# Performance work log

Hardware: AMD Instinct MI355X
Metric: run time of the kernel (lower is better)

The kernel has to match this reference:

```python
import jax, jax.numpy as jnp
import numpy as np

B, S, D, H, E = 2, 2048, 1024, 2048, 8
TOP_K = 2
AUX_COEF = 0.01


def setup_inputs() -> dict:
    key = jax.random.key(0)
    ks = jax.random.split(key, 5)
    x = jax.random.normal(ks[0], (B, S, D), jnp.float32)
    Wr = jax.random.normal(ks[1], (E, D), jnp.float32) * 0.02   # router: Linear(D, E) weight [E, D]
    W1 = jax.random.normal(ks[2], (E, H, D), jnp.float32) * 0.02  # per-expert Linear(D, H)
    W2 = jax.random.normal(ks[3], (E, D, H), jnp.float32) * 0.02  # per-expert Linear(H, D)
    W3 = jax.random.normal(ks[4], (E, H, D), jnp.float32) * 0.02  # per-expert Linear(D, H)
    return {"x": x, "Wr": Wr, "W1": W1, "W2": W2, "W3": W3}


def reference(x, Wr, W1, W2, W3):
    b, s, d = x.shape
    e = Wr.shape[0]
    xf = x.reshape(-1, d)                               # [N, D]
    logits = xf @ Wr.T                                  # [N, E]
    probs = jax.nn.softmax(logits, axis=-1)
    _, topk_idx = jax.lax.top_k(logits, TOP_K)          # indices from logits (as in torch code)
    topk_probs, _ = jax.lax.top_k(probs, TOP_K)         # values from probs (same order; softmax monotone)
    # aux loss: density of top-1 expert * mean router prob
    density = jnp.mean(jax.nn.one_hot(topk_idx[:, 0], e, dtype=xf.dtype), axis=0)
    aux_loss = AUX_COEF * jnp.sum(density * probs.mean(axis=0)) * e
    # combine gates: gate[n, j] = sum_i topk_probs[n,i] * 1[topk_idx[n,i]==j]
    gates = jnp.sum(jax.nn.one_hot(topk_idx, e, dtype=xf.dtype) * topk_probs[..., None], axis=1)  # [N, E]
    # dense per-expert SwiGLU; masked combine gives identical math to gather/scatter loop
    h = jax.nn.silu(jnp.einsum('nd,ehd->enh', xf, W1)) * jnp.einsum('nd,ehd->enh', xf, W3)  # [E, N, H]
    y = jnp.einsum('enh,edh->end', h, W2)               # [E, N, D]
    out = jnp.einsum('ne,end->nd', gates, y)            # [N, D]
    return out.reshape(b, s, d), aux_loss
```

## Files before the change

kernel.cpp:

```cpp
#include <hip/hip_runtime.h>
#include <stdint.h>

#define NTOK 4096
#define DD 1024
#define HH 2048
#define NE 8
#define CAP 4096

typedef short bf16x8 __attribute__((ext_vector_type(8)));
typedef float f32x4 __attribute__((ext_vector_type(4)));
typedef unsigned short u16;
typedef unsigned int u32;

__device__ __forceinline__ u16 f2b(float f){
    union { float f; u32 u; } v; v.f = f;
    return (u16)((v.u + 0x7fffu + ((v.u >> 16) & 1u)) >> 16);
}
__device__ __forceinline__ float b2f(u16 h){
    union { u32 u; float f; } v; v.u = ((u32)h) << 16;
    return v.f;
}
__device__ __forceinline__ u32 pk2(float a, float b){
    return (u32)f2b(a) | ((u32)f2b(b) << 16);
}
__device__ __forceinline__ void gload16(const u16* g, u16* l){
    __builtin_amdgcn_global_load_lds((const __attribute__((address_space(1))) u32*)g,
                                     (__attribute__((address_space(3))) u32*)l, 16, 0, 0);
}
__device__ __forceinline__ int prefix_off(const int* __restrict__ cnt, int e){
    int o = 0;
    #pragma unroll
    for (int i = 0; i < NE; ++i) if (i < e) o += cnt[i];
    return o;
}

__global__ __launch_bounds__(256) void prep_kernel(const float* __restrict__ x,
        const float* __restrict__ Wr,
        const float* __restrict__ W1, const float* __restrict__ W3,
        u16* __restrict__ xb, u16* __restrict__ w1b, u16* __restrict__ w3b,
        int* __restrict__ cnt, int* __restrict__ list,
        float* __restrict__ glist, float* __restrict__ psum,
        int* __restrict__ cnt1, int* __restrict__ islot){
    __shared__ float wS[NE * DD];
    __shared__ float psumS[NE];
    __shared__ int cnt1S[NE], cntS[NE], baseS[NE];
    __shared__ int tE[32], tL[32];
    __shared__ float tP[32];
    int tid = threadIdx.x;
    int bid = blockIdx.x;

    if (bid >= 256){
        int cb = bid - 256;
        int m = cb >> 10, blk = cb & 1023;
        const float* s = (m == 0) ? W1 : W3;
        u16* d = (m == 0) ? w1b : w3b;
        int base = blk * 4096 + tid;
        #pragma unroll 4
        for (int j = 0; j < 16; ++j){
            int i = base + j * 256;
            float4 v = reinterpret_cast<const float4*>(s)[i];
            ushort4 o; o.x = f2b(v.x); o.y = f2b(v.y); o.z = f2b(v.z); o.w = f2b(v.w);
            reinterpret_cast<ushort4*>(d)[i] = o;
        }
        return;
    }

    for (int i = tid; i < NE * DD / 4; i += 256)
        reinterpret_cast<float4*>(wS)[i] = reinterpret_cast<const float4*>(Wr)[i];
    if (tid < NE){ psumS[tid] = 0.f; cnt1S[tid] = 0; cntS[tid] = 0; }
    __syncthreads();
    int lane = tid & 63, w = tid >> 6;
    for (int t = 0; t < 4; ++t){
        int li = w * 4 + t;
        int n = bid * 16 + li;
        const float4* xr = reinterpret_cast<const float4*>(x + (size_t)n * DD);
        ushort4* xbr = reinterpret_cast<ushort4*>(xb + (size_t)n * DD);
        float acc[NE];
        #pragma unroll
        for (int e = 0; e < NE; ++e) acc[e] = 0.f;
        #pragma unroll
        for (int j = 0; j < 4; ++j){
            float4 xv = xr[lane + 64 * j];
            ushort4 xo; xo.x = f2b(xv.x); xo.y = f2b(xv.y); xo.z = f2b(xv.z); xo.w = f2b(xv.w);
            xbr[lane + 64 * j] = xo;
            #pragma unroll
            for (int e = 0; e < NE; ++e){
                float4 wv = reinterpret_cast<const float4*>(wS + e * DD)[lane + 64 * j];
                acc[e] += xv.x * wv.x + xv.y * wv.y + xv.z * wv.z + xv.w * wv.w;
            }
        }
        #pragma unroll
        for (int e = 0; e < NE; ++e){
            float v = acc[e];
            #pragma unroll
            for (int s = 32; s > 0; s >>= 1) v += __shfl_xor(v, s);
            acc[e] = v;
        }
        if (lane == 0){
            float mx = acc[0];
            #pragma unroll
            for (int e = 1; e < NE; ++e) mx = fmaxf(mx, acc[e]);
            float p[NE], sm = 0.f;
            #pragma unroll
            for (int e = 0; e < NE; ++e){ p[e] = expf(acc[e] - mx); sm += p[e]; }
            float inv = 1.f / sm;
            #pragma unroll
            for (int e = 0; e < NE; ++e){ p[e] *= inv; atomicAdd(&psumS[e], p[e]); }
            int i0 = 0;
            #pragma unroll
            for (int e = 1; e < NE; ++e) if (acc[e] > acc[i0]) i0 = e;
            int i1 = -1;
            #pragma unroll
            for (int e = 0; e < NE; ++e) if (e != i0 && (i1 < 0 || acc[e] > acc[i1])) i1 = e;
            atomicAdd(&cnt1S[i0], 1);
            int l0 = atomicAdd(&cntS[i0], 1);
            int l1 = atomicAdd(&cntS[i1], 1);
            tE[li * 2] = i0; tE[li * 2 + 1] = i1;
            tP[li * 2] = p[i0]; tP[li * 2 + 1] = p[i1];
            tL[li * 2] = l0; tL[li * 2 + 1] = l1;
        }
    }
    __syncthreads();
    if (tid < NE){
        baseS[tid] = atomicAdd(&cnt[tid], cntS[tid]);
        atomicAdd(&psum[tid], psumS[tid]);
        atomicAdd(&cnt1[tid], cnt1S[tid]);
    }
    __syncthreads();
    if (tid < 32){
        int e = tE[tid], pos = baseS[e] + tL[tid];
        int n = bid * 16 + (tid >> 1);
        list[e * CAP + pos]  = n;
        glist[e * CAP + pos] = tP[tid];
        islot[n * 2 + (tid & 1)] = e * CAP + pos;
    }
}

__global__ __launch_bounds__(256, 3) void ffn1_kernel(const u16* __restrict__ xb,
        const u16* __restrict__ w1b, const u16* __restrict__ w3b,
        const float* __restrict__ W2f, u16* __restrict__ w2b,
        const int* __restrict__ cnt, const int* __restrict__ list,
        u16* __restrict__ hbuf){
    int bid = blockIdx.x;
    int tid = threadIdx.x;

    if (bid >= 768){
        int cb = bid - 768;
        int base = cb * 4096 + tid;
        #pragma unroll 4
        for (int j = 0; j < 16; ++j){
            int i = base + j * 256;
            float4 v = reinterpret_cast<const float4*>(W2f)[i];
            ushort4 o; o.x = f2b(v.x); o.y = f2b(v.y); o.z = f2b(v.z); o.w = f2b(v.w);
            reinterpret_cast<ushort4*>(w2b)[i] = o;
        }
        return;
    }

    int e = bid & 7;
    int slot = bid >> 3;
    int rows = cnt[e];
    int hoff = prefix_off(cnt, e);
    int n0 = (slot & 31) * 64;

    __shared__ u16 aS[128 * 64];
    __shared__ u16 bS[128 * 64];

    int lane = tid & 63, w = tid >> 6;
    int wm = (w & 1) * 64, wn = (w >> 1) * 32;
    int fr = lane & 15, fg = lane >> 4, fr7 = fr & 7;
    int rc = lane >> 3, ce = ((lane & 7) ^ rc) * 8;

    const u16* bptr[4];
    #pragma unroll
    for (int q = 0; q < 4; ++q){
        int br = (w * 4 + q) * 8 + rc;
        const u16* wb = (br < 64) ? w1b : w3b;
        bptr[q] = wb + ((size_t)e * HH + n0 + (br & 63)) * DD + ce;
    }
    u16* aL = aS + w * 4 * 512;
    u16* bL = bS + w * 4 * 512;

    for (int mt = slot >> 5; mt < 32; mt += 3){
        int m0 = mt << 7;
        if (m0 >= rows) break;

        const u16* aptr[4];
        #pragma unroll
        for (int q = 0; q < 4; ++q){
            int r = m0 + (w * 4 + q) * 8 + rc;
            int tok = list[e * CAP + (r < rows ? r : rows - 1)];
            aptr[q] = xb + (size_t)tok * DD + ce;
        }

        f32x4 acc1[4][2], acc3[4][2];
        #pragma unroll
        for (int mi = 0; mi < 4; ++mi)
            #pragma unroll
            for (int ni = 0; ni < 2; ++ni)
                #pragma unroll
                for (int j = 0; j < 4; ++j){ acc1[mi][ni][j] = 0.f; acc3[mi][ni][j] = 0.f; }

        for (int k0 = 0; k0 < DD; k0 += 64){
            #pragma unroll
            for (int q = 0; q < 4; ++q){
                gload16(aptr[q] + k0, aL + q * 512);
                gload16(bptr[q] + k0, bL + q * 512);
            }
            __syncthreads();
            #pragma unroll
            for (int ks = 0; ks < 2; ++ks){
                int sl = ((ks * 4 + fg) ^ fr7) * 8;
                bf16x8 a[4], b1[2], b3[2];
                #pragma unroll
                for (int mi = 0; mi < 4; ++mi)
                    a[mi] = *reinterpret_cast<const bf16x8*>(&aS[(wm + mi * 16 + fr) * 64 + sl]);
                #pragma unroll
                for (int ni = 0; ni < 2; ++ni){
                    b1[ni] = *reinterpret_cast<const bf16x8*>(&bS[(wn + ni * 16 + fr) * 64 + sl]);
                    b3[ni] = *reinterpret_cast<const bf16x8*>(&bS[(64 + wn + ni * 16 + fr) * 64 + sl]);
                }
                #pragma unroll
                for (int mi = 0; mi < 4; ++mi)
                    #pragma unroll
                    for (int ni = 0; ni < 2; ++ni){
                        acc1[mi][ni] = __builtin_amdgcn_mfma_f32_16x16x32_bf16(a[mi], b1[ni], acc1[mi][ni], 0, 0, 0);
                        acc3[mi][ni] = __builtin_amdgcn_mfma_f32_16x16x32_bf16(a[mi], b3[ni], acc3[mi][ni], 0, 0, 0);
                    }
            }
            __syncthreads();
        }

        #pragma unroll
        for (int mi = 0; mi < 4; ++mi)
            #pragma unroll
            for (int ni = 0; ni < 2; ++ni)
                #pragma unroll
                for (int j = 0; j < 4; ++j){
                    int r = wm + mi * 16 + fg * 4 + j;
                    int tr = m0 + r;
                    if (tr < rows){
                        int c = n0 + wn + ni * 16 + fr;
                        float v1 = acc1[mi][ni][j], v3 = acc3[mi][ni][j];
                        float hv = (v1 / (1.f + expf(-v1))) * v3;
                        hbuf[(size_t)(hoff + tr) * HH + c] = f2b(hv);
                    }
                }
    }
}

__global__ __launch_bounds__(256, 3) void ffn2_kernel(const u16* __restrict__ hbuf,
        const u16* __restrict__ w2b, const int* __restrict__ cnt,
        u16* __restrict__ ybuf){
    int bid = blockIdx.x;
    int e = bid & 7;
    int slot = bid >> 3;
    int rows = cnt[e];
    int hoff = prefix_off(cnt, e);
    int n0 = (slot & 7) * 128;

    __shared__ u16 aS[128 * 64];
    __shared__ u16 bS[128 * 64];

    int tid = threadIdx.x, lane = tid & 63, w = tid >> 6;
    int wm = (w & 1) * 64, wn = (w >> 1) * 64;
    int fr = lane & 15, fg = lane >> 4, fr7 = fr & 7;
    int rc = lane >> 3, ce = ((lane & 7) ^ rc) * 8;

    const u16* bp = w2b + ((size_t)e * DD + n0 + w * 32 + rc) * HH + ce;
    u16* aL = aS + w * 4 * 512;
    u16* bL = bS + w * 4 * 512;

    for (int mt = slot >> 3; mt < 32; mt += 12){
        int m0 = mt << 7;
        if (m0 >= rows) break;

        const u16* aptr[4];
        #pragma unroll
        for (int q = 0; q < 4; ++q){
            int r = m0 + (w * 4 + q) * 8 + rc;
            if (r >= rows) r = rows - 1;
            aptr[q] = hbuf + (size_t)(hoff + r) * HH + ce;
        }

        f32x4 acc[4][4];
        #pragma unroll
        for (int mi = 0; mi < 4; ++mi)
            #pragma unroll
            for (int ni = 0; ni < 4; ++ni)
                #pragma unroll
                for (int j = 0; j < 4; ++j) acc[mi][ni][j] = 0.f;

        for (int k0 = 0; k0 < HH; k0 += 64){
            #pragma unroll
            for (int q = 0; q < 4; ++q){
                gload16(aptr[q] + k0, aL + q * 512);
                gload16(bp + q * 8 * HH + k0, bL + q * 512);
            }
            __syncthreads();
            #pragma unroll
            for (int ks = 0; ks < 2; ++ks){
                int sl = ((ks * 4 + fg) ^ fr7) * 8;
                bf16x8 a[4], b[4];
                #pragma unroll
                for (int mi = 0; mi < 4; ++mi)
                    a[mi] = *reinterpret_cast<const bf16x8*>(&aS[(wm + mi * 16 + fr) * 64 + sl]);
                #pragma unroll
                for (int ni = 0; ni < 4; ++ni)
                    b[ni] = *reinterpret_cast<const bf16x8*>(&bS[(wn + ni * 16 + fr) * 64 + sl]);
                #pragma unroll
                for (int mi = 0; mi < 4; ++mi)
                    #pragma unroll
                    for (int ni = 0; ni < 4; ++ni)
                        acc[mi][ni] = __builtin_amdgcn_mfma_f32_16x16x32_bf16(a[mi], b[ni], acc[mi][ni], 0, 0, 0);
            }
            __syncthreads();
        }

        #pragma unroll
        for (int mi = 0; mi < 4; ++mi)
            #pragma unroll
            for (int ni = 0; ni < 4; ++ni)
                #pragma unroll
                for (int j = 0; j < 4; ++j){
                    int r = wm + mi * 16 + fg * 4 + j;
                    int tr = m0 + r;
                    if (tr < rows){
                        int c = wn + ni * 16 + fr;
                        ybuf[(size_t)(hoff + tr) * DD + n0 + c] = f2b(acc[mi][ni][j]);
                    }
                }
    }
}

__global__ __launch_bounds__(256, 2) void ffn1_small(const u16* __restrict__ xb,
        const float* __restrict__ W1f, const float* __restrict__ W3f,
        const int* __restrict__ cnt, const int* __restrict__ list,
        u16* __restrict__ hbuf){
    int bid = blockIdx.x;
    int widx = (bid & 7) * 512 + (bid >> 3);
    int e = widx >> 9, n0t = (widx >> 5) & 15, mt = widx & 31;
    int rows = cnt[e];
    int m0 = mt * 128;
    if (m0 >= rows) return;
    int n0 = n0t * 128;
    int hoff = prefix_off(cnt, e);
    __shared__ u16 aS[128 * 64];
    __shared__ u16 b1S[128 * 64];
    __shared__ u16 b3S[128 * 64];
    int tid = threadIdx.x, lane = tid & 63, w = tid >> 6;
    int wm = (w & 1) * 64, wn = (w >> 1) * 64;
    int fr = lane & 15, fg = lane >> 4, fr7 = fr & 7;
    int rc = lane >> 3, ce = ((lane & 7) ^ rc) * 8;
    const u16* aptr[4];
    #pragma unroll
    for (int q = 0; q < 4; ++q){
        int r = m0 + (w * 4 + q) * 8 + rc;
        int tok = list[e * CAP + (r < rows ? r : rows - 1)];
        aptr[q] = xb + (size_t)tok * DD + ce;
    }
    size_t brw = (size_t)(e * HH + n0 + w * 32 + rc) * DD + ce;
    const float* b1pf = W1f + brw;
    const float* b3pf = W3f + brw;
    u16* aL  = aS  + w * 4 * 512;
    u16* b1L = b1S + w * 4 * 512;
    u16* b3L = b3S + w * 4 * 512;
    f32x4 acc1[4][4], acc3[4][4];
    #pragma unroll
    for (int mi = 0; mi < 4; ++mi)
        #pragma unroll
        for (int ni = 0; ni < 4; ++ni)
            #pragma unroll
            for (int j = 0; j < 4; ++j){ acc1[mi][ni][j] = 0.f; acc3[mi][ni][j] = 0.f; }
    for (int k0 = 0; k0 < DD; k0 += 64){
        #pragma unroll
        for (int q = 0; q < 4; ++q){
            gload16(aptr[q] + k0, aL + q * 512);
            const float* s1 = b1pf + q * 8 * DD + k0;
            float4 f0 = reinterpret_cast<const float4*>(s1)[0];
            float4 f1 = reinterpret_cast<const float4*>(s1)[1];
            int4 v; v.x = pk2(f0.x,f0.y); v.y = pk2(f0.z,f0.w); v.z = pk2(f1.x,f1.y); v.w = pk2(f1.z,f1.w);
            *reinterpret_cast<int4*>(b1L + q * 512 + lane * 8) = v;
            const float* s3 = b3pf + q * 8 * DD + k0;
            float4 g0 = reinterpret_cast<const float4*>(s3)[0];
            float4 g1 = reinterpret_cast<const float4*>(s3)[1];
            int4 u; u.x = pk2(g0.x,g0.y); u.y = pk2(g0.z,g0.w); u.z = pk2(g1.x,g1.y); u.w = pk2(g1.z,g1.w);
            *reinterpret_cast<int4*>(b3L + q * 512 + lane * 8) = u;
        }
        __syncthreads();
        #pragma unroll
        for (int ks = 0; ks < 2; ++ks){
            int sl = ((ks * 4 + fg) ^ fr7) * 8;
            bf16x8 a[4], b1[4], b3[4];
            #pragma unroll
            for (int mi = 0; mi < 4; ++mi)
                a[mi] = *reinterpret_cast<const bf16x8*>(&aS[(wm + mi * 16 + fr) * 64 + sl]);
            #pragma unroll
            for (int ni = 0; ni < 4; ++ni){
                b1[ni] = *reinterpret_cast<const bf16x8*>(&b1S[(wn + ni * 16 + fr) * 64 + sl]);
                b3[ni] = *reinterpret_cast<const bf16x8*>(&b3S[(wn + ni * 16 + fr) * 64 + sl]);
            }
            #pragma unroll
            for (int mi = 0; mi < 4; ++mi)
                #pragma unroll
                for (int ni = 0; ni < 4; ++ni){
                    acc1[mi][ni] = __builtin_amdgcn_mfma_f32_16x16x32_bf16(a[mi], b1[ni], acc1[mi][ni], 0, 0, 0);
                    acc3[mi][ni] = __builtin_amdgcn_mfma_f32_16x16x32_bf16(a[mi], b3[ni], acc3[mi][ni], 0, 0, 0);
                }
        }
        __syncthreads();
    }
    #pragma unroll
    for (int mi = 0; mi < 4; ++mi)
        #pragma unroll
        for (int ni = 0; ni < 4; ++ni)
            #pragma unroll
            for (int j = 0; j < 4; ++j){
                int r = wm + mi * 16 + fg * 4 + j;
                int tr = m0 + r;
                if (tr < rows){
                    int c = wn + ni * 16 + fr;
                    float v1 = acc1[mi][ni][j], v3 = acc3[mi][ni][j];
                    float hv = (v1 / (1.f + expf(-v1))) * v3;
                    hbuf[(size_t)(hoff + tr) * HH + n0 + c] = f2b(hv);
                }
            }
}

__global__ __launch_bounds__(256, 2) void ffn2_small(const u16* __restrict__ hbuf,
        const float* __restrict__ W2f, const int* __restrict__ cnt,
        u16* __restrict__ ybuf){
    int bid = blockIdx.x;
    int widx = (bid & 7) * 256 + (bid >> 3);
    int e = widx >> 8, n0t = (widx >> 5) & 7, mt = widx & 31;
    int rows = cnt[e];
    int m0 = mt * 128;
    if (m0 >= rows) return;
    int n0 = n0t * 128;
    int hoff = prefix_off(cnt, e);
    __shared__ u16 aS[128 * 64];
    __shared__ u16 bS[128 * 64];
    int tid = threadIdx.x, lane = tid & 63, w = tid >> 6;
    int wm = (w & 1) * 64, wn = (w >> 1) * 64;
    int fr = lane & 15, fg = lane >> 4, fr7 = fr & 7;
    int rc = lane >> 3, ce = ((lane & 7) ^ rc) * 8;
    const u16* aptr[4];
    #pragma unroll
    for (int q = 0; q < 4; ++q){
        int r = m0 + (w * 4 + q) * 8 + rc;
        if (r >= rows) r = rows - 1;
        aptr[q] = hbuf + (size_t)(hoff + r) * HH + ce;
    }
    const float* b2pf = W2f + (size_t)(e * DD + n0 + w * 32 + rc) * HH + ce;
    u16* aL = aS + w * 4 * 512;
    u16* bL = bS + w * 4 * 512;
    f32x4 acc[4][4];
    #pragma unroll
    for (int mi = 0; mi < 4; ++mi)
        #pragma unroll
        for (int ni = 0; ni < 4; ++ni)
            #pragma unroll
            for (int j = 0; j < 4; ++j) acc[mi][ni][j] = 0.f;
    for (int k0 = 0; k0 < HH; k0 += 64){
        #pragma unroll
        for (int q = 0; q < 4; ++q){
            gload16(aptr[q] + k0, aL + q * 512);
            const float* s2 = b2pf + q * 8 * HH + k0;
            float4 f0 = reinterpret_cast<const float4*>(s2)[0];
            float4 f1 = reinterpret_cast<const float4*>(s2)[1];
            int4 v; v.x = pk2(f0.x,f0.y); v.y = pk2(f0.z,f0.w); v.z = pk2(f1.x,f1.y); v.w = pk2(f1.z,f1.w);
            *reinterpret_cast<int4*>(bL + q * 512 + lane * 8) = v;
        }
        __syncthreads();
        #pragma unroll
        for (int ks = 0; ks < 2; ++ks){
            int sl = ((ks * 4 + fg) ^ fr7) * 8;
            bf16x8 a[4], b[4];
            #pragma unroll
            for (int mi = 0; mi < 4; ++mi)
                a[mi] = *reinterpret_cast<const bf16x8*>(&aS[(wm + mi * 16 + fr) * 64 + sl]);
            #pragma unroll
            for (int ni = 0; ni < 4; ++ni)
                b[ni] = *reinterpret_cast<const bf16x8*>(&bS[(wn + ni * 16 + fr) * 64 + sl]);
            #pragma unroll
            for (int mi = 0; mi < 4; ++mi)
                #pragma unroll
                for (int ni = 0; ni < 4; ++ni)
                    acc[mi][ni] = __builtin_amdgcn_mfma_f32_16x16x32_bf16(a[mi], b[ni], acc[mi][ni], 0, 0, 0);
        }
        __syncthreads();
    }
    #pragma unroll
    for (int mi = 0; mi < 4; ++mi)
        #pragma unroll
        for (int ni = 0; ni < 4; ++ni)
            #pragma unroll
            for (int j = 0; j < 4; ++j){
                int r = wm + mi * 16 + fg * 4 + j;
                int tr = m0 + r;
                if (tr < rows){
                    int c = wn + ni * 16 + fr;
                    ybuf[(size_t)(hoff + tr) * DD + n0 + c] = f2b(acc[mi][ni][j]);
                }
            }
}

__global__ __launch_bounds__(256) void combine_kernel(const u16* __restrict__ ybuf,
        const int* __restrict__ islot, const int* __restrict__ cnt,
        const float* __restrict__ glist, const float* __restrict__ psum,
        const int* __restrict__ cnt1, float* __restrict__ out){
    int idx = blockIdx.x * 256 + threadIdx.x;
    if (idx == 0){
        float aux = 0.f;
        #pragma unroll
        for (int e = 0; e < NE; ++e)
            aux += ((float)cnt1[e] * (1.f / NTOK)) * (psum[e] * (1.f / NTOK));
        out[(size_t)NTOK * DD] = 0.01f * aux * (float)NE;
    }
    int n = idx >> 7, c = (idx & 127) * 8;
    int id0 = islot[n * 2], id1 = islot[n * 2 + 1];
    int r0 = prefix_off(cnt, id0 >> 12) + (id0 & 4095);
    int r1 = prefix_off(cnt, id1 >> 12) + (id1 & 4095);
    float g0 = glist[id0], g1 = glist[id1];
    ushort4 y0a = reinterpret_cast<const ushort4*>(ybuf + (size_t)r0 * DD + c)[0];
    ushort4 y0b = reinterpret_cast<const ushort4*>(ybuf + (size_t)r0 * DD + c)[1];
    ushort4 y1a = reinterpret_cast<const ushort4*>(ybuf + (size_t)r1 * DD + c)[0];
    ushort4 y1b = reinterpret_cast<const ushort4*>(ybuf + (size_t)r1 * DD + c)[1];
    float4 o0, o1;
    o0.x = g0 * b2f(y0a.x) + g1 * b2f(y1a.x);
    o0.y = g0 * b2f(y0a.y) + g1 * b2f(y1a.y);
    o0.z = g0 * b2f(y0a.z) + g1 * b2f(y1a.z);
    o0.w = g0 * b2f(y0a.w) + g1 * b2f(y1a.w);
    o1.x = g0 * b2f(y0b.x) + g1 * b2f(y1b.x);
    o1.y = g0 * b2f(y0b.y) + g1 * b2f(y1b.y);
    o1.z = g0 * b2f(y0b.z) + g1 * b2f(y1b.z);
    o1.w = g0 * b2f(y0b.w) + g1 * b2f(y1b.w);
    float4* op = reinterpret_cast<float4*>(out + (size_t)n * DD + c);
    op[0] = o0; op[1] = o1;
}

extern "C" void kernel_launch(void* const* d_in, const int* in_sizes, int n_in,
                              void* d_out, int out_size, void* d_ws, size_t ws_size,
                              hipStream_t stream) {
    const float* x  = (const float*)d_in[0];
    const float* Wr = (const float*)d_in[1];
    const float* W1 = (const float*)d_in[2];
    const float* W2 = (const float*)d_in[3];
    const float* W3 = (const float*)d_in[4];
    float* out = (float*)d_out;

    char* wp = (char*)d_ws;
    u16*   hbuf  = (u16*)  (wp);
    u16*   xb    = (u16*)  (wp + 33554432);
    int*   list  = (int*)  (wp + 41943040);
    float* glist = (float*)(wp + 42074112);
    int*   cnt   = (int*)  (wp + 42205184);
    float* psum  = (float*)(wp + 42205216);
    int*   cnt1  = (int*)  (wp + 42205248);
    int*   islot = (int*)  (wp + 42205312);
    const size_t WOFF = 42238208;
    const size_t WB   = 33554432;
    u16* w1b = (u16*)(wp + WOFF);
    u16* w2b = (u16*)(wp + WOFF + WB);
    u16* w3b = (u16*)(wp + WOFF + 2 * WB);
    u16* ybuf = (u16*)(wp + WOFF);
    const size_t NEED_FULL = WOFF + 3 * WB;
    bool bw = ws_size >= NEED_FULL;

    hipMemsetAsync(wp + 42205184, 0, 128, stream);

    prep_kernel<<<bw ? 2304 : 256, 256, 0, stream>>>(
        x, Wr, W1, W3, xb, w1b, w3b, cnt, list, glist, psum, cnt1, islot);
    if (bw){
        ffn1_kernel<<<1792, 256, 0, stream>>>(xb, w1b, w3b, W2, w2b, cnt, list, hbuf);
        ffn2_kernel<<<768, 256, 0, stream>>>(hbuf, w2b, cnt, ybuf);
    } else {
        ffn1_small<<<4096, 256, 0, stream>>>(xb, W1, W3, cnt, list, hbuf);
        ffn2_small<<<2048, 256, 0, stream>>>(hbuf, W2, cnt, ybuf);
    }
    combine_kernel<<<NTOK * (DD / 8) / 256, 256, 0, stream>>>(
        ybuf, islot, cnt, glist, psum, cnt1, out);
}
```

Before: 196.6 us.

## Double-buffer LDS tiles in ffn1 and cut resident blocks to two per CU

The ffn1 GEMM main loop now uses two LDS buffers, prefetching the tile two steps ahead with vmcnt-based waits and raw barriers, so global-to-LDS loads overlap MFMA work. LDS doubles to 64KB per block, so launch bounds drop to 2 blocks per CU. The m-tile stride and the W2 conversion block offset change from 3 to 2 slots (768 to 512), which shrinks the grid. In exchange, fewer waves are resident to hide latency, and the hand-written vmcnt counts depend on how the compiler emits gload16.

Result: slower. 210.2 us (+6.9%).

```diff
diff --git a/kernel.cpp b/kernel.cpp
--- a/kernel.cpp
+++ b/kernel.cpp
@@ -136,7 +136,7 @@
     }
 }
 
-__global__ __launch_bounds__(256, 3) void ffn1_kernel(const u16* __restrict__ xb,
+__global__ __launch_bounds__(256, 2) void ffn1_kernel(const u16* __restrict__ xb,
         const u16* __restrict__ w1b, const u16* __restrict__ w3b,
         const float* __restrict__ W2f, u16* __restrict__ w2b,
         const int* __restrict__ cnt, const int* __restrict__ list,
@@ -144,8 +144,8 @@
     int bid = blockIdx.x;
     int tid = threadIdx.x;
 
-    if (bid >= 768){
-        int cb = bid - 768;
+    if (bid >= 512){
+        int cb = bid - 512;
         int base = cb * 4096 + tid;
         #pragma unroll 4
         for (int j = 0; j < 16; ++j){
@@ -163,8 +163,8 @@
     int hoff = prefix_off(cnt, e);
     int n0 = (slot & 31) * 64;
 
-    __shared__ u16 aS[128 * 64];
-    __shared__ u16 bS[128 * 64];
+    __shared__ u16 aS[2][128 * 64];
+    __shared__ u16 bS[2][128 * 64];
 
     int lane = tid & 63, w = tid >> 6;
     int wm = (w & 1) * 64, wn = (w >> 1) * 32;
@@ -178,10 +178,9 @@
         const u16* wb = (br < 64) ? w1b : w3b;
         bptr[q] = wb + ((size_t)e * HH + n0 + (br & 63)) * DD + ce;
     }
-    u16* aL = aS + w * 4 * 512;
-    u16* bL = bS + w * 4 * 512;
-
-    for (int mt = slot >> 5; mt < 32; mt += 3){
+    int ldso = w * 4 * 512;
+
+    for (int mt = slot >> 5; mt < 32; mt += 2){
         int m0 = mt << 7;
         if (m0 >= rows) break;
 
@@ -201,24 +200,35 @@
                 #pragma unroll
                 for (int j = 0; j < 4; ++j){ acc1[mi][ni][j] = 0.f; acc3[mi][ni][j] = 0.f; }
 
-        for (int k0 = 0; k0 < DD; k0 += 64){
+        auto STAGE = [&](int buf, int kofs){
             #pragma unroll
             for (int q = 0; q < 4; ++q){
-                gload16(aptr[q] + k0, aL + q * 512);
-                gload16(bptr[q] + k0, bL + q * 512);
-            }
-            __syncthreads();
+                gload16(aptr[q] + kofs, aS[buf] + ldso + q * 512);
+                gload16(bptr[q] + kofs, bS[buf] + ldso + q * 512);
+            }
+        };
+
+        const int NT = DD / 64;
+        STAGE(0, 0);
+        STAGE(1, 64);
+        asm volatile("s_waitcnt vmcnt(8)" ::: "memory");
+        __builtin_amdgcn_s_barrier();
+
+        for (int t = 0; t < NT; ++t){
+            int cur = t & 1;
+            const u16* Ac = aS[cur];
+            const u16* Bc = bS[cur];
             #pragma unroll
             for (int ks = 0; ks < 2; ++ks){
                 int sl = ((ks * 4 + fg) ^ fr7) * 8;
                 bf16x8 a[4], b1[2], b3[2];
                 #pragma unroll
                 for (int mi = 0; mi < 4; ++mi)
-                    a[mi] = *reinterpret_cast<const bf16x8*>(&aS[(wm + mi * 16 + fr) * 64 + sl]);
+                    a[mi] = *reinterpret_cast<const bf16x8*>(&Ac[(wm + mi * 16 + fr) * 64 + sl]);
                 #pragma unroll
                 for (int ni = 0; ni < 2; ++ni){
-                    b1[ni] = *reinterpret_cast<const bf16x8*>(&bS[(wn + ni * 16 + fr) * 64 + sl]);
-                    b3[ni] = *reinterpret_cast<const bf16x8*>(&bS[(64 + wn + ni * 16 + fr) * 64 + sl]);
+                    b1[ni] = *reinterpret_cast<const bf16x8*>(&Bc[(wn + ni * 16 + fr) * 64 + sl]);
+                    b3[ni] = *reinterpret_cast<const bf16x8*>(&Bc[(64 + wn + ni * 16 + fr) * 64 + sl]);
                 }
                 #pragma unroll
                 for (int mi = 0; mi < 4; ++mi)
@@ -228,7 +238,14 @@
                         acc3[mi][ni] = __builtin_amdgcn_mfma_f32_16x16x32_bf16(a[mi], b3[ni], acc3[mi][ni], 0, 0, 0);
                     }
             }
-            __syncthreads();
+            __builtin_amdgcn_s_barrier();
+            if (t + 2 < NT){
+                STAGE(cur, (t + 2) * 64);
+                asm volatile("s_waitcnt vmcnt(8)" ::: "memory");
+            } else {
+                asm volatile("s_waitcnt vmcnt(0)" ::: "memory");
+            }
+            __builtin_amdgcn_s_barrier();
         }
 
         #pragma unroll
@@ -572,7 +589,7 @@
     prep_kernel<<<bw ? 2304 : 256, 256, 0, stream>>>(
         x, Wr, W1, W3, xb, w1b, w3b, cnt, list, glist, psum, cnt1, islot);
     if (bw){
-        ffn1_kernel<<<1792, 256, 0, stream>>>(xb, w1b, w3b, W2, w2b, cnt, list, hbuf);
+        ffn1_kernel<<<1536, 256, 0, stream>>>(xb, w1b, w3b, W2, w2b, cnt, list, hbuf);
         ffn2_kernel<<<768, 256, 0, stream>>>(hbuf, w2b, cnt, ybuf);
     } else {
         ffn1_small<<<4096, 256, 0, stream>>>(xb, W1, W3, cnt, list, hbuf);
```

## Restructure ffn1 into 256x256 tiles with double-buffered LDS and interleaved MFMA phases

Applied to the files above, without the earlier changes.

The ffn1 expert GEMM moves from 256-thread blocks with 128x128 tiles (W1 and W3 halves) to 512-thread blocks with 256x256 tiles. It double-buffers the A and B shared-memory tiles and splits each k-step into four MFMA phases, issuing the next loads between barriers with explicit vmcnt waits and raised s_setprio around the MFMAs. The aim is to hide global-load latency and raise data reuse per LDS load. The cost is 128 KB of LDS per block and much higher register pressure, which limits occupancy. The W2 conversion tail blocks are resized to the new block shape.

Measured after the change: 221.8 us. +12.8%, slower.

```diff
diff --git a/kernel.cpp b/kernel.cpp
--- a/kernel.cpp
+++ b/kernel.cpp
@@ -136,7 +136,7 @@
     }
 }
 
-__global__ __launch_bounds__(256, 3) void ffn1_kernel(const u16* __restrict__ xb,
+__global__ __launch_bounds__(512, 2) void ffn1_kernel(const u16* __restrict__ xb,
         const u16* __restrict__ w1b, const u16* __restrict__ w3b,
         const float* __restrict__ W2f, u16* __restrict__ w2b,
         const int* __restrict__ cnt, const int* __restrict__ list,
@@ -144,12 +144,12 @@
     int bid = blockIdx.x;
     int tid = threadIdx.x;
 
-    if (bid >= 768){
-        int cb = bid - 768;
+    if (bid >= 512){
+        int cb = bid - 512;
         int base = cb * 4096 + tid;
         #pragma unroll 4
-        for (int j = 0; j < 16; ++j){
-            int i = base + j * 256;
+        for (int j = 0; j < 8; ++j){
+            int i = base + j * 512;
             float4 v = reinterpret_cast<const float4*>(W2f)[i];
             ushort4 o; o.x = f2b(v.x); o.y = f2b(v.y); o.z = f2b(v.z); o.w = f2b(v.w);
             reinterpret_cast<ushort4*>(w2b)[i] = o;
@@ -157,93 +157,177 @@
         return;
     }
 
+    __shared__ u16 aS[2 * 256 * 64];
+    __shared__ u16 bS[2 * 256 * 64];
+
     int e = bid & 7;
     int slot = bid >> 3;
+    int n0t = slot & 15, mtg = slot >> 4;
     int rows = cnt[e];
     int hoff = prefix_off(cnt, e);
-    int n0 = (slot & 31) * 64;
-
-    __shared__ u16 aS[128 * 64];
-    __shared__ u16 bS[128 * 64];
+    int n0g = n0t * 128;
 
     int lane = tid & 63, w = tid >> 6;
-    int wm = (w & 1) * 64, wn = (w >> 1) * 32;
+    int wr = w >> 2, wc = w & 3;
     int fr = lane & 15, fg = lane >> 4, fr7 = fr & 7;
-    int rc = lane >> 3, ce = ((lane & 7) ^ rc) * 8;
-
-    const u16* bptr[4];
-    #pragma unroll
-    for (int q = 0; q < 4; ++q){
-        int br = (w * 4 + q) * 8 + rc;
-        const u16* wb = (br < 64) ? w1b : w3b;
-        bptr[q] = wb + ((size_t)e * HH + n0 + (br & 63)) * DD + ce;
-    }
-    u16* aL = aS + w * 4 * 512;
-    u16* bL = bS + w * 4 * 512;
-
-    for (int mt = slot >> 5; mt < 32; mt += 3){
-        int m0 = mt << 7;
+    int sr = tid >> 3;
+    int ce2 = ((tid & 7) ^ (sr & 7)) * 8;
+
+    const u16* bp[4];
+    #pragma unroll
+    for (int c = 0; c < 4; ++c){
+        int br = c * 64 + sr;
+        int which = (br >> 4) & 1;
+        int wcol = n0g + (br >> 5) * 16 + (br & 15);
+        bp[c] = (which ? w3b : w1b) + ((size_t)e * HH + wcol) * DD + ce2;
+    }
+    int arow = wr * 128 + fr;
+    int brow = wc * 64 + fr;
+
+    for (int mt = mtg; mt < 16; mt += 4){
+        int m0 = mt << 8;
         if (m0 >= rows) break;
 
-        const u16* aptr[4];
-        #pragma unroll
-        for (int q = 0; q < 4; ++q){
-            int r = m0 + (w * 4 + q) * 8 + rc;
+        const u16* ap[4];
+        #pragma unroll
+        for (int c = 0; c < 4; ++c){
+            int r = m0 + c * 64 + sr;
             int tok = list[e * CAP + (r < rows ? r : rows - 1)];
-            aptr[q] = xb + (size_t)tok * DD + ce;
-        }
-
-        f32x4 acc1[4][2], acc3[4][2];
-        #pragma unroll
-        for (int mi = 0; mi < 4; ++mi)
+            ap[c] = xb + (size_t)tok * DD + ce2;
+        }
+
+        f32x4 acc[8][4];
+        #pragma unroll
+        for (int mi = 0; mi < 8; ++mi)
+            #pragma unroll
+            for (int ni = 0; ni < 4; ++ni)
+                #pragma unroll
+                for (int j = 0; j < 4; ++j) acc[mi][ni][j] = 0.f;
+
+        auto SA = [&](int buf, int c, int k){
+            gload16(ap[c] + k, aS + buf * 16384 + c * 4096 + tid * 8);
+        };
+        auto SB = [&](int buf, int c, int k){
+            gload16(bp[c] + k, bS + buf * 16384 + c * 4096 + tid * 8);
+        };
+
+        #pragma unroll
+        for (int c = 0; c < 4; ++c) SA(0, c, 0);
+        #pragma unroll
+        for (int c = 0; c < 4; ++c) SB(0, c, 0);
+        #pragma unroll
+        for (int c = 0; c < 4; ++c) SA(1, c, 64);
+        asm volatile("s_waitcnt vmcnt(4)" ::: "memory");
+        asm volatile("s_barrier" ::: "memory");
+
+        for (int t = 0; t < 16; ++t){
+            int cur = t & 1;
+            const u16* Ac = aS + cur * 16384;
+            const u16* Bc = bS + cur * 16384;
+            bf16x8 a[4][2], b[2][2];
+
+            #pragma unroll
+            for (int mi = 0; mi < 4; ++mi)
+                #pragma unroll
+                for (int ks = 0; ks < 2; ++ks)
+                    a[mi][ks] = *(const bf16x8*)&Ac[(arow + mi * 16) * 64 + (((ks * 4 + fg) ^ fr7) * 8)];
             #pragma unroll
             for (int ni = 0; ni < 2; ++ni)
                 #pragma unroll
-                for (int j = 0; j < 4; ++j){ acc1[mi][ni][j] = 0.f; acc3[mi][ni][j] = 0.f; }
-
-        for (int k0 = 0; k0 < DD; k0 += 64){
-            #pragma unroll
-            for (int q = 0; q < 4; ++q){
-                gload16(aptr[q] + k0, aL + q * 512);
-                gload16(bptr[q] + k0, bL + q * 512);
-            }
-            __syncthreads();
-            #pragma unroll
-            for (int ks = 0; ks < 2; ++ks){
-                int sl = ((ks * 4 + fg) ^ fr7) * 8;
-                bf16x8 a[4], b1[2], b3[2];
-                #pragma unroll
-                for (int mi = 0; mi < 4; ++mi)
-                    a[mi] = *reinterpret_cast<const bf16x8*>(&aS[(wm + mi * 16 + fr) * 64 + sl]);
-                #pragma unroll
-                for (int ni = 0; ni < 2; ++ni){
-                    b1[ni] = *reinterpret_cast<const bf16x8*>(&bS[(wn + ni * 16 + fr) * 64 + sl]);
-                    b3[ni] = *reinterpret_cast<const bf16x8*>(&bS[(64 + wn + ni * 16 + fr) * 64 + sl]);
-                }
+                for (int ks = 0; ks < 2; ++ks)
+                    b[ni][ks] = *(const bf16x8*)&Bc[(brow + ni * 16) * 64 + (((ks * 4 + fg) ^ fr7) * 8)];
+            if (t + 1 < 16){
+                #pragma unroll
+                for (int c = 0; c < 4; ++c) SB(cur ^ 1, c, (t + 1) * 64);
+            }
+            asm volatile("s_barrier" ::: "memory");
+            __builtin_amdgcn_s_setprio(1);
+            #pragma unroll
+            for (int ks = 0; ks < 2; ++ks)
                 #pragma unroll
                 for (int mi = 0; mi < 4; ++mi)
                     #pragma unroll
-                    for (int ni = 0; ni < 2; ++ni){
-                        acc1[mi][ni] = __builtin_amdgcn_mfma_f32_16x16x32_bf16(a[mi], b1[ni], acc1[mi][ni], 0, 0, 0);
-                        acc3[mi][ni] = __builtin_amdgcn_mfma_f32_16x16x32_bf16(a[mi], b3[ni], acc3[mi][ni], 0, 0, 0);
-                    }
-            }
-            __syncthreads();
-        }
-
-        #pragma unroll
-        for (int mi = 0; mi < 4; ++mi)
+                    for (int ni = 0; ni < 2; ++ni)
+                        acc[mi][ni] = __builtin_amdgcn_mfma_f32_16x16x32_bf16(a[mi][ks], b[ni][ks], acc[mi][ni], 0, 0, 0);
+            __builtin_amdgcn_s_setprio(0);
+            asm volatile("s_barrier" ::: "memory");
+
             #pragma unroll
             for (int ni = 0; ni < 2; ++ni)
                 #pragma unroll
+                for (int ks = 0; ks < 2; ++ks)
+                    b[ni][ks] = *(const bf16x8*)&Bc[(brow + 32 + ni * 16) * 64 + (((ks * 4 + fg) ^ fr7) * 8)];
+            if (t + 2 < 16){ SA(cur, 0, (t + 2) * 64); SA(cur, 2, (t + 2) * 64); }
+            asm volatile("s_barrier" ::: "memory");
+            __builtin_amdgcn_s_setprio(1);
+            #pragma unroll
+            for (int ks = 0; ks < 2; ++ks)
+                #pragma unroll
+                for (int mi = 0; mi < 4; ++mi)
+                    #pragma unroll
+                    for (int ni = 0; ni < 2; ++ni)
+                        acc[mi][2 + ni] = __builtin_amdgcn_mfma_f32_16x16x32_bf16(a[mi][ks], b[ni][ks], acc[mi][2 + ni], 0, 0, 0);
+            __builtin_amdgcn_s_setprio(0);
+            asm volatile("s_barrier" ::: "memory");
+
+            #pragma unroll
+            for (int mi = 0; mi < 4; ++mi)
+                #pragma unroll
+                for (int ks = 0; ks < 2; ++ks)
+                    a[mi][ks] = *(const bf16x8*)&Ac[(arow + 64 + mi * 16) * 64 + (((ks * 4 + fg) ^ fr7) * 8)];
+            #pragma unroll
+            for (int ni = 0; ni < 2; ++ni)
+                #pragma unroll
+                for (int ks = 0; ks < 2; ++ks)
+                    b[ni][ks] = *(const bf16x8*)&Bc[(brow + ni * 16) * 64 + (((ks * 4 + fg) ^ fr7) * 8)];
+            asm volatile("s_barrier" ::: "memory");
+            __builtin_amdgcn_s_setprio(1);
+            #pragma unroll
+            for (int ks = 0; ks < 2; ++ks)
+                #pragma unroll
+                for (int mi = 0; mi < 4; ++mi)
+                    #pragma unroll
+                    for (int ni = 0; ni < 2; ++ni)
+                        acc[4 + mi][ni] = __builtin_amdgcn_mfma_f32_16x16x32_bf16(a[mi][ks], b[ni][ks], acc[4 + mi][ni], 0, 0, 0);
+            __builtin_amdgcn_s_setprio(0);
+            asm volatile("s_barrier" ::: "memory");
+
+            #pragma unroll
+            for (int ni = 0; ni < 2; ++ni)
+                #pragma unroll
+                for (int ks = 0; ks < 2; ++ks)
+                    b[ni][ks] = *(const bf16x8*)&Bc[(brow + 32 + ni * 16) * 64 + (((ks * 4 + fg) ^ fr7) * 8)];
+            if (t + 2 < 16){
+                SA(cur, 1, (t + 2) * 64); SA(cur, 3, (t + 2) * 64);
+                asm volatile("s_waitcnt vmcnt(4)" ::: "memory");
+            } else if (t + 1 < 16){
+                asm volatile("s_waitcnt vmcnt(0)" ::: "memory");
+            }
+            asm volatile("s_barrier" ::: "memory");
+            __builtin_amdgcn_s_setprio(1);
+            #pragma unroll
+            for (int ks = 0; ks < 2; ++ks)
+                #pragma unroll
+                for (int mi = 0; mi < 4; ++mi)
+                    #pragma unroll
+                    for (int ni = 0; ni < 2; ++ni)
+                        acc[4 + mi][2 + ni] = __builtin_amdgcn_mfma_f32_16x16x32_bf16(a[mi][ks], b[ni][ks], acc[4 + mi][2 + ni], 0, 0, 0);
+            __builtin_amdgcn_s_setprio(0);
+            asm volatile("s_barrier" ::: "memory");
+        }
+
+        #pragma unroll
+        for (int mi = 0; mi < 8; ++mi)
+            #pragma unroll
+            for (int P = 0; P < 2; ++P)
+                #pragma unroll
                 for (int j = 0; j < 4; ++j){
-                    int r = wm + mi * 16 + fg * 4 + j;
-                    int tr = m0 + r;
-                    if (tr < rows){
-                        int c = n0 + wn + ni * 16 + fr;
-                        float v1 = acc1[mi][ni][j], v3 = acc3[mi][ni][j];
+                    int r = m0 + wr * 128 + mi * 16 + fg * 4 + j;
+                    if (r < rows){
+                        int col = n0g + (wc * 2 + P) * 16 + fr;
+                        float v1 = acc[mi][P * 2][j], v3 = acc[mi][P * 2 + 1][j];
                         float hv = (v1 / (1.f + expf(-v1))) * v3;
-                        hbuf[(size_t)(hoff + tr) * HH + c] = f2b(hv);
+                        hbuf[(size_t)(hoff + r) * HH + col] = f2b(hv);
                     }
                 }
     }
@@ -572,7 +656,7 @@
     prep_kernel<<<bw ? 2304 : 256, 256, 0, stream>>>(
         x, Wr, W1, W3, xb, w1b, w3b, cnt, list, glist, psum, cnt1, islot);
     if (bw){
-        ffn1_kernel<<<1792, 256, 0, stream>>>(xb, w1b, w3b, W2, w2b, cnt, list, hbuf);
+        ffn1_kernel<<<1536, 512, 0, stream>>>(xb, w1b, w3b, W2, w2b, cnt, list, hbuf);
         ffn2_kernel<<<768, 256, 0, stream>>>(hbuf, w2b, cnt, ybuf);
     } else {
         ffn1_small<<<4096, 256, 0, stream>>>(xb, W1, W3, cnt, list, hbuf);
```
